# Kernel tuning notes

Hardware: AMD Instinct MI355X
Metric: run time of the kernel (lower is better)

## Reference

```python
import jax, jax.numpy as jnp
import numpy as np

N_QUBITS = 4 + 4  # 8
N_LAYERS = 4
DIM = 2 ** N_QUBITS


def _apply_1q(state, U, wire):
    # state: (B, 2,...,2) complex; U: (2,2) complex; contract qubit `wire`
    s = jnp.moveaxis(state, wire + 1, -1)
    s = s @ U.T  # out[..., i] = sum_j U[i, j] * s[..., j]
    return jnp.moveaxis(s, -1, wire + 1)


def _apply_cnot(state, c, t):
    s = jnp.moveaxis(state, (c + 1, t + 1), (-2, -1))  # (..., 2c, 2t)
    s = jnp.concatenate([s[..., 0:1, :], s[..., 1:2, ::-1]], axis=-2)
    return jnp.moveaxis(s, (-2, -1), (c + 1, t + 1))


def _quantum_layer(q_in, qw):
    """Batched statevector sim: RY(pi*x) encoding + StronglyEntanglingLayers + <Z_i>."""
    B = q_in.shape[0]
    # RY(a)|0> = cos(a/2)|0> + sin(a/2)|1>, a = pi * x  -> product state
    half = q_in * (jnp.pi / 2)
    qvecs = jnp.stack([jnp.cos(half), jnp.sin(half)], axis=-1).astype(jnp.complex64)  # (B, n, 2)
    state = qvecs[:, 0]
    for i in range(1, N_QUBITS):
        state = (state[:, :, None] * qvecs[:, i][:, None, :]).reshape(B, -1)
    state = state.reshape((B,) + (2,) * N_QUBITS)
    # Rot(phi, theta, omega) = RZ(omega) RY(theta) RZ(phi)
    phi, theta, omega = qw[..., 0], qw[..., 1], qw[..., 2]
    c, s = jnp.cos(theta / 2), jnp.sin(theta / 2)
    m00 = jnp.exp(-0.5j * (phi + omega)) * c
    m01 = -jnp.exp(0.5j * (phi - omega)) * s
    m10 = jnp.exp(-0.5j * (phi - omega)) * s
    m11 = jnp.exp(0.5j * (phi + omega)) * c
    rot = jnp.stack([jnp.stack([m00, m01], -1), jnp.stack([m10, m11], -1)], -2)  # (L, n, 2, 2)
    rot = rot.astype(jnp.complex64)
    for l in range(N_LAYERS):
        for w in range(N_QUBITS):
            state = _apply_1q(state, rot[l, w], w)
        r = (l % (N_QUBITS - 1)) + 1  # PennyLane default ranges
        for w in range(N_QUBITS):
            state = _apply_cnot(state, w, (w + r) % N_QUBITS)
    amps = state.reshape(B, DIM)
    probs = jnp.real(amps * jnp.conj(amps))  # (B, 2^n) float32
    # <Z_i> = sum_b probs_b * (+1 if bit_i(b)==0 else -1); wire 0 = most significant axis
    idx = np.arange(DIM)
    bits = (idx[None, :] >> (N_QUBITS - 1 - np.arange(N_QUBITS))[:, None]) & 1  # (n, 2^n)
    zvals = jnp.asarray(1.0 - 2.0 * bits, dtype=jnp.float32)
    return probs @ zvals.T  # (B, n)


def _forward(x, w_pre1, b_pre1, w_pre2, b_pre2, w_pre3, b_pre3, qw,
             w_post1, b_post1, w_post2, b_post2, w_post3, b_post3):
    # eval mode: dropout is identity
    h = jax.nn.relu(x @ w_pre1 + b_pre1)
    h = jax.nn.relu(h @ w_pre2 + b_pre2)
    q_in = jnp.tanh(h @ w_pre3 + b_pre3)          # (B, n_qubits)
    z = _quantum_layer(q_in, qw)                   # (B, n_qubits)
    h = jax.nn.relu(z @ w_post1 + b_post1)
    h = jax.nn.relu(h @ w_post2 + b_post2)
    return h @ w_post3 + b_post3                   # (B, num_classes)


def setup_inputs() -> dict:
    key = jax.random.key(0)
    ks = jax.random.split(key, 16)
    B, D_IN, C = 16384, 41, 5
    def lin(k, fan_in, fan_out):
        lim = 1.0 / np.sqrt(fan_in)
        k1, k2 = jax.random.split(k)
        return (jax.random.uniform(k1, (fan_in, fan_out), jnp.float32, -lim, lim),
                jax.random.uniform(k2, (fan_out,), jnp.float32, -lim, lim))
    x = jax.random.normal(ks[0], (B, D_IN), jnp.float32)
    w_pre1, b_pre1 = lin(ks[1], D_IN, 64)
    w_pre2, b_pre2 = lin(ks[2], 64, 32)
    w_pre3, b_pre3 = lin(ks[3], 32, N_QUBITS)
    qw = jax.random.normal(ks[4], (N_LAYERS, N_QUBITS, 3), jnp.float32) * 0.1
    w_post1, b_post1 = lin(ks[5], N_QUBITS, 32)
    w_post2, b_post2 = lin(ks[6], 32, 16)
    w_post3, b_post3 = lin(ks[7], 16, C)
    return dict(x=x, w_pre1=w_pre1, b_pre1=b_pre1, w_pre2=w_pre2, b_pre2=b_pre2,
                w_pre3=w_pre3, b_pre3=b_pre3, qw=qw,
                w_post1=w_post1, b_post1=b_post1, w_post2=w_post2, b_post2=b_post2,
                w_post3=w_post3, b_post3=b_post3)


def reference(x, w_pre1, b_pre1, w_pre2, b_pre2, w_pre3, b_pre3, qw,
              w_post1, b_post1, w_post2, b_post2, w_post3, b_post3):
    return _forward(x, w_pre1, b_pre1, w_pre2, b_pre2, w_pre3, b_pre3, qw,
                    w_post1, b_post1, w_post2, b_post2, w_post3, b_post3)
```

## Files before the change

kernel.cpp:

```cpp
#include <hip/hip_runtime.h>
#include <math.h>

#define PI_HALF 1.57079632679489662f

typedef float v2f __attribute__((ext_vector_type(2)));
typedef _Float16 h8 __attribute__((ext_vector_type(8)));
typedef _Float16 h2v __attribute__((ext_vector_type(2)));
typedef float f4 __attribute__((ext_vector_type(4)));


__device__ __forceinline__ v2f sp(float x) { v2f r; r.x = x; r.y = x; return r; }
__device__ __forceinline__ v2f pkfma(v2f a, v2f b, v2f c) {
  return __builtin_elementwise_fma(a, b, c);
}

template <int CTRL>
__device__ __forceinline__ float dpp_mov(float v) {
  int r = __builtin_amdgcn_update_dpp(0, __float_as_int(v), CTRL, 0xf, 0xf, true);
  return __int_as_float(r);
}
template <int CTRL, int ROW, int BANK>
__device__ __forceinline__ float mdpp(float old_, float src) {
  int r = __builtin_amdgcn_update_dpp(__float_as_int(old_), __float_as_int(src),
                                      CTRL, ROW, BANK, false);
  return __int_as_float(r);
}
template <int MASK>
__device__ __forceinline__ float lane_xor(float v) {
  if constexpr (MASK == 1) return dpp_mov<0xB1>(v);
  else if constexpr (MASK == 2) return dpp_mov<0x4E>(v);
  else if constexpr (MASK == 8) return dpp_mov<0x128>(v);
  else return dpp_mov<0x1B>(dpp_mov<0x141>(v));
}
template <int MASK>
__device__ __forceinline__ v2f dpp2(v2f v) {
  v2f r; r.x = lane_xor<MASK>(v.x); r.y = lane_xor<MASK>(v.y); return r;
}

template <int W>
__device__ __forceinline__ void rot_lane(v2f (&RE)[8], v2f (&IM)[8],
                                         const float4 mA, int g) {
  constexpr int LM = 1 << (3 - W);
  const unsigned bit = (g >> (3 - W)) & 1u;
  const int sgn = (int)(bit << 31);
  v2f Av = sp(mA.x);
  v2f Bv = sp(__int_as_float(__float_as_int(mA.y) ^ sgn));
  v2f Cv = sp(__int_as_float(__float_as_int(mA.z) ^ sgn));
  v2f Dv = sp(mA.w);
#pragma unroll
  for (int j = 0; j < 8; ++j) {
    v2f pr = dpp2<LM>(RE[j]);
    v2f pi = dpp2<LM>(IM[j]);
    v2f nr = pkfma(-Dv, pi, pkfma(Cv, pr, pkfma(-Bv, IM[j], Av * RE[j])));
    v2f ni = pkfma( Dv, pr, pkfma(Cv, pi, pkfma( Bv, RE[j], Av * IM[j])));
    RE[j] = nr; IM[j] = ni;
  }
}
template <int JM>
__device__ __forceinline__ void rot_regj(v2f (&RE)[8], v2f (&IM)[8],
                                         const float4 mA) {
  v2f M0r = sp(mA.x), M0i = sp(mA.y), M1r = sp(mA.z), M1i = sp(mA.w);
#pragma unroll
  for (int j = 0; j < 8; ++j) {
    if (!(j & JM)) {
      const int j1 = j | JM;
      v2f r0 = RE[j], i0 = IM[j], r1 = RE[j1], i1 = IM[j1];
      RE[j]  = pkfma(-M1i, i1, pkfma(M1r, r1, pkfma(-M0i, i0, M0r * r0)));
      IM[j]  = pkfma( M1i, r1, pkfma(M1r, i1, pkfma( M0i, r0, M0r * i0)));
      RE[j1] = pkfma( M0i, i1, pkfma(M0r, r1, pkfma(-M1i, i0, (-M1r) * r0)));
      IM[j1] = pkfma(-M0i, r1, pkfma(M0r, i1, pkfma( M1i, r0, (-M1r) * i0)));
    }
  }
}
__device__ __forceinline__ void rot_regh(v2f (&RE)[8], v2f (&IM)[8],
                                         const float4 mA) {
#pragma unroll
  for (int j = 0; j < 8; ++j) {
    float r0 = RE[j].x, i0 = IM[j].x, r1 = RE[j].y, i1 = IM[j].y;
    RE[j].x = fmaf(-mA.w, i1, fmaf(mA.z, r1, fmaf(-mA.y, i0, mA.x * r0)));
    IM[j].x = fmaf( mA.w, r1, fmaf(mA.z, i1, fmaf( mA.y, r0, mA.x * i0)));
    RE[j].y = fmaf( mA.y, i1, fmaf(mA.x, r1, fmaf(-mA.w, i0, -mA.z * r0)));
    IM[j].y = fmaf(-mA.y, r1, fmaf(mA.x, i1, fmaf( mA.w, r0, -mA.z * i0)));
  }
}
template <int GPOS, int LM>
__device__ __forceinline__ void cnot_LL(v2f (&RE)[8], v2f (&IM)[8], int g) {
  if constexpr (GPOS >= 2) {
    constexpr int BANK = (GPOS == 3) ? 0xC : 0xA;
    if constexpr (LM == 4) {
#pragma unroll
      for (int j = 0; j < 8; ++j) {
        float t0 = dpp_mov<0x141>(RE[j].x);
        float t1 = dpp_mov<0x141>(RE[j].y);
        float t2 = dpp_mov<0x141>(IM[j].x);
        float t3 = dpp_mov<0x141>(IM[j].y);
        RE[j].x = mdpp<0x1B, 0xF, BANK>(RE[j].x, t0);
        RE[j].y = mdpp<0x1B, 0xF, BANK>(RE[j].y, t1);
        IM[j].x = mdpp<0x1B, 0xF, BANK>(IM[j].x, t2);
        IM[j].y = mdpp<0x1B, 0xF, BANK>(IM[j].y, t3);
      }
    } else {
      constexpr int CTRL = (LM == 1) ? 0xB1 : (LM == 2) ? 0x4E : 0x128;
#pragma unroll
      for (int j = 0; j < 8; ++j) {
        RE[j].x = mdpp<CTRL, 0xF, BANK>(RE[j].x, RE[j].x);
        RE[j].y = mdpp<CTRL, 0xF, BANK>(RE[j].y, RE[j].y);
        IM[j].x = mdpp<CTRL, 0xF, BANK>(IM[j].x, IM[j].x);
        IM[j].y = mdpp<CTRL, 0xF, BANK>(IM[j].y, IM[j].y);
      }
    }
  } else {
    constexpr int CTRL =
        (GPOS == 1 && LM == 1) ? 0xB4 :
        (GPOS == 1 && LM == 2) ? 0x44 :
        (GPOS == 0 && LM == 1) ? 0xA0 :
                                 0x6C;
#pragma unroll
    for (int j = 0; j < 8; ++j) {
      RE[j].x = dpp_mov<CTRL>(RE[j].x);
      RE[j].y = dpp_mov<CTRL>(RE[j].y);
      IM[j].x = dpp_mov<CTRL>(IM[j].x);
      IM[j].y = dpp_mov<CTRL>(IM[j].y);
    }
  }
}
template <int GPOS, int JM>
__device__ __forceinline__ void cnot_LR(v2f (&RE)[8], v2f (&IM)[8], int g) {
  const bool cb = (g >> GPOS) & 1;
#pragma unroll
  for (int j = 0; j < 8; ++j) {
    if (!(j & JM)) {
      const int j1 = j | JM;
      v2f r0 = RE[j], r1 = RE[j1];
      RE[j] = cb ? r1 : r0;  RE[j1] = cb ? r0 : r1;
      v2f i0 = IM[j], i1 = IM[j1];
      IM[j] = cb ? i1 : i0;  IM[j1] = cb ? i0 : i1;
    }
  }
}
template <int GPOS>
__device__ __forceinline__ void cnot_LH(v2f (&RE)[8], v2f (&IM)[8], int g) {
  const bool cb = (g >> GPOS) & 1;
#pragma unroll
  for (int j = 0; j < 8; ++j) {
    v2f r = RE[j]; v2f rs; rs.x = r.y; rs.y = r.x;
    RE[j] = cb ? rs : r;
    v2f i = IM[j]; v2f is2; is2.x = i.y; is2.y = i.x;
    IM[j] = cb ? is2 : i;
  }
}
template <int JC, int LM>
__device__ __forceinline__ void cnot_RL(v2f (&RE)[8], v2f (&IM)[8]) {
#pragma unroll
  for (int j = 0; j < 8; ++j) {
    if (j & JC) {
      RE[j] = dpp2<LM>(RE[j]);
      IM[j] = dpp2<LM>(IM[j]);
    }
  }
}
template <int JC>
__device__ __forceinline__ void cnot_RH(v2f (&RE)[8], v2f (&IM)[8]) {
#pragma unroll
  for (int j = 0; j < 8; ++j) {
    if (j & JC) {
      v2f r = RE[j]; RE[j].x = r.y; RE[j].y = r.x;
      v2f i = IM[j]; IM[j].x = i.y; IM[j].y = i.x;
    }
  }
}
template <int LM>
__device__ __forceinline__ void cnot_HL(v2f (&RE)[8], v2f (&IM)[8]) {
#pragma unroll
  for (int j = 0; j < 8; ++j) {
    RE[j].y = lane_xor<LM>(RE[j].y);
    IM[j].y = lane_xor<LM>(IM[j].y);
  }
}
template <int JC, int JT>
__device__ __forceinline__ void cnot_RR(v2f (&RE)[8], v2f (&IM)[8]) {
#pragma unroll
  for (int j = 0; j < 8; ++j) {
    if ((j & JC) && !(j & JT)) {
      const int j1 = j | JT;
      v2f t = RE[j]; RE[j] = RE[j1]; RE[j1] = t;
      t = IM[j]; IM[j] = IM[j1]; IM[j1] = t;
    }
  }
}

__device__ __forceinline__ void stage_fence() { __threadfence_block(); }

#define CIRCUIT_BODY(RE, IM, g)                                        \
  ROTS(0)                                                              \
  cnot_LL<3, 4>(RE, IM, g);  cnot_LL<2, 2>(RE, IM, g);                 \
  cnot_LL<1, 1>(RE, IM, g);  cnot_LR<0, 4>(RE, IM, g);                 \
  cnot_RR<4, 2>(RE, IM);     cnot_RR<2, 1>(RE, IM);                    \
  cnot_RH<1>(RE, IM);        cnot_HL<8>(RE, IM);                       \
  ROTS(1)                                                              \
  cnot_LL<3, 2>(RE, IM, g);  cnot_LL<2, 1>(RE, IM, g);                 \
  cnot_LR<1, 4>(RE, IM, g);  cnot_LR<0, 2>(RE, IM, g);                 \
  cnot_RR<4, 1>(RE, IM);     cnot_RH<2>(RE, IM);                       \
  cnot_RL<1, 8>(RE, IM);     cnot_HL<4>(RE, IM);                       \
  ROTS(2)                                                              \
  cnot_LL<3, 1>(RE, IM, g);  cnot_LR<2, 4>(RE, IM, g);                 \
  cnot_LR<1, 2>(RE, IM, g);  cnot_LR<0, 1>(RE, IM, g);                 \
  cnot_RH<4>(RE, IM);        cnot_RL<2, 8>(RE, IM);                    \
  cnot_RL<1, 4>(RE, IM);     cnot_HL<2>(RE, IM);                       \
  ROTS(3)                                                              \
  cnot_LR<3, 4>(RE, IM, g);  cnot_LR<2, 2>(RE, IM, g);                 \
  cnot_LR<1, 1>(RE, IM, g);  cnot_LH<0>(RE, IM, g);                    \
  cnot_RL<4, 8>(RE, IM);     cnot_RL<2, 4>(RE, IM);                    \
  cnot_RL<1, 2>(RE, IM);     cnot_HL<1>(RE, IM);

__global__ __launch_bounds__(256) void build_u_kernel(
    const float* __restrict__ qw, _Float16* __restrict__ Btf) {
  __shared__ __align__(16) float rotm[32][4];
  const int tid = threadIdx.x;
  const int g = tid & 15;
  const int ls = tid >> 4;
  const int c = blockIdx.x * 16 + ls;

  if (tid < 32) {
    float phi = qw[tid * 3 + 0];
    float th  = qw[tid * 3 + 1];
    float om  = qw[tid * 3 + 2];
    float st_, ct; sincosf(0.5f * th, &st_, &ct);
    float sa, ca;  sincosf(0.5f * (phi + om), &sa, &ca);
    float sb, cb;  sincosf(0.5f * (phi - om), &sb, &cb);
    rotm[tid][0] =  ca * ct;
    rotm[tid][1] = -sa * ct;
    rotm[tid][2] = -cb * st_;
    rotm[tid][3] = -sb * st_;
  }
  __syncthreads();

  v2f RE[8], IM[8];
#pragma unroll
  for (int j = 0; j < 8; ++j) {
    RE[j].x = (c == g * 16 + 2 * j)     ? 1.0f : 0.0f;
    RE[j].y = (c == g * 16 + 2 * j + 1) ? 1.0f : 0.0f;
    IM[j] = sp(0.0f);
  }

#define RM(L, W) (*(const float4*)(&rotm[(L) * 8 + (W)][0]))
#define ROTS(L)                                                          \
  {                                                                      \
    float4 c0 = RM(L, 0), c1 = RM(L, 1), c2 = RM(L, 2), c3 = RM(L, 3),   \
           c4 = RM(L, 4), c5 = RM(L, 5), c6 = RM(L, 6), c7 = RM(L, 7);   \
    rot_lane<0>(RE, IM, c0, g);                                          \
    rot_lane<1>(RE, IM, c1, g);                                          \
    rot_lane<2>(RE, IM, c2, g);                                          \
    rot_lane<3>(RE, IM, c3, g);                                          \
    rot_regj<4>(RE, IM, c4);                                             \
    rot_regj<2>(RE, IM, c5);                                             \
    rot_regj<1>(RE, IM, c6);                                             \
    rot_regh(RE, IM, c7);                                                \
  }
  CIRCUIT_BODY(RE, IM, g)
#undef ROTS
#undef RM

  {
    const int kt = c >> 5;
    const int rg = (c >> 3) & 3;
    const int e  = c & 7;
    const int baseR = ((g * 2 + 0) * 8 + kt) * 512 + rg * 128 + e;
    const int baseI = ((g * 2 + 1) * 8 + kt) * 512 + rg * 128 + e;
#pragma unroll
    for (int j = 0; j < 8; ++j) {
      Btf[baseR + (2 * j) * 8]     = (_Float16)RE[j].x;
      Btf[baseR + (2 * j + 1) * 8] = (_Float16)RE[j].y;
      Btf[baseI + (2 * j) * 8]     = (_Float16)IM[j].x;
      Btf[baseI + (2 * j + 1) * 8] = (_Float16)IM[j].y;
    }
  }
}

__global__ __launch_bounds__(256) void hqc_main(
    const float* __restrict__ x,
    const float* __restrict__ w1, const float* __restrict__ b1,
    const float* __restrict__ w2, const float* __restrict__ b2,
    const float* __restrict__ w3, const float* __restrict__ b3,
    const _Float16* __restrict__ Btf,
    const float* __restrict__ wp1, const float* __restrict__ bp1,
    const float* __restrict__ wp2, const float* __restrict__ bp2,
    const float* __restrict__ wp3, const float* __restrict__ bp3,
    float* __restrict__ out, int B) {
  __shared__ __align__(16) _Float16 A_half[4096];
  __shared__ __align__(16) float R1[16][44];
  __shared__ __align__(16) float R2[16][68];

  const int tid = threadIdx.x;
  const int g = tid & 15;
  const int ls = tid >> 4;
  const int s = blockIdx.x * 16 + ls;
  const bool valid = (s < B);

  if (valid) {
    R1[ls][g]      = x[s * 41 + g];
    R1[ls][g + 16] = x[s * 41 + g + 16];
    if (g < 9) R1[ls][g + 32] = x[s * 41 + g + 32];
  }
  stage_fence();

  {
    const float4* w1v = (const float4*)w1;
    float4 bv = ((const float4*)b1)[g];
    v2f aA; aA.x = bv.x; aA.y = bv.y;
    v2f aB; aB.x = bv.z; aB.y = bv.w;
#pragma unroll 8
    for (int k = 0; k < 41; ++k) {
      float xk = R1[ls][k];
      float4 wv = w1v[k * 16 + g];
      v2f w01; w01.x = wv.x; w01.y = wv.y;
      v2f w23; w23.x = wv.z; w23.y = wv.w;
      v2f xv = sp(xk);
      aA = pkfma(xv, w01, aA);
      aB = pkfma(xv, w23, aB);
    }
    float4 st4;
    st4.x = fmaxf(aA.x, 0.f); st4.y = fmaxf(aA.y, 0.f);
    st4.z = fmaxf(aB.x, 0.f); st4.w = fmaxf(aB.y, 0.f);
    *(float4*)(&R2[ls][4 * g]) = st4;
  }
  stage_fence();

  {
    const v2f* w2v = (const v2f*)w2;
    v2f a2 = ((const v2f*)b2)[g];
#pragma unroll 8
    for (int k = 0; k < 64; ++k)
      a2 = pkfma(sp(R2[ls][k]), w2v[k * 16 + g], a2);
    R1[ls][2 * g]     = fmaxf(a2.x, 0.f);
    R1[ls][2 * g + 1] = fmaxf(a2.y, 0.f);
  }
  stage_fence();

  if (g < 8) {
    float acc = b3[g];
#pragma unroll
    for (int k = 0; k < 32; ++k) acc = fmaf(R1[ls][k], w3[k * 8 + g], acc);
    float q = tanhf(acc);
    float sh, ch; sincosf(q * PI_HALF, &sh, &ch);
    R2[ls][g]     = ch;
    R2[ls][8 + g] = sh;
  }
  stage_fence();

  {
    float cwv[8], swv[8];
#pragma unroll
    for (int w = 0; w < 8; ++w) { cwv[w] = R2[ls][w]; swv[w] = R2[ls][8 + w]; }
    float lp = 1.0f;
#pragma unroll
    for (int w = 0; w < 4; ++w) lp *= ((g >> (3 - w)) & 1) ? swv[w] : cwv[w];
    float f45[4];
#pragma unroll
    for (int a = 0; a < 4; ++a)
      f45[a] = ((a & 2) ? swv[4] : cwv[4]) * ((a & 1) ? swv[5] : cwv[5]);
    v2f F67[2];
    F67[0].x = cwv[6] * cwv[7]; F67[0].y = cwv[6] * swv[7];
    F67[1].x = swv[6] * cwv[7]; F67[1].y = swv[6] * swv[7];
#pragma unroll
    for (int j = 0; j < 8; ++j) {
      v2f amp = sp(lp * f45[j >> 1]) * F67[j & 1];
      h2v pk; pk.x = (_Float16)amp.x; pk.y = (_Float16)amp.y;
      const int k = g * 16 + 2 * j;
      const int addr = ((k >> 5) * 4 + ((k >> 3) & 3)) * 128 + ls * 8 + (k & 7);
      *(h2v*)(&A_half[addr]) = pk;
    }
  }
  __syncthreads();

  {
    const int l = tid & 63;
    const int w = tid >> 6;

    f4 accr[4], acci[4];
#pragma unroll
    for (int t = 0; t < 4; ++t) {
      accr[t] = (f4){0.f, 0.f, 0.f, 0.f};
      acci[t] = (f4){0.f, 0.f, 0.f, 0.f};
    }
    const _Float16* Arow = &A_half[l * 8];
    const _Float16* Bre[4];
    const _Float16* Bim[4];
#pragma unroll
    for (int t = 0; t < 4; ++t) {
      const int p = w + 4 * t;
      Bre[t] = Btf + ((p * 2 + 0) * 8) * 512 + l * 8;
      Bim[t] = Btf + ((p * 2 + 1) * 8) * 512 + l * 8;
    }

#pragma unroll
    for (int kt = 0; kt < 8; ++kt) {
      h8 av = *(const h8*)(Arow + kt * 512);
      h8 br0 = *(const h8*)(Bre[0] + kt * 512);
      h8 bi0 = *(const h8*)(Bim[0] + kt * 512);
      h8 br1 = *(const h8*)(Bre[1] + kt * 512);
      h8 bi1 = *(const h8*)(Bim[1] + kt * 512);
      h8 br2 = *(const h8*)(Bre[2] + kt * 512);
      h8 bi2 = *(const h8*)(Bim[2] + kt * 512);
      h8 br3 = *(const h8*)(Bre[3] + kt * 512);
      h8 bi3 = *(const h8*)(Bim[3] + kt * 512);
      accr[0] = __builtin_amdgcn_mfma_f32_16x16x32_f16(av, br0, accr[0], 0, 0, 0);
      acci[0] = __builtin_amdgcn_mfma_f32_16x16x32_f16(av, bi0, acci[0], 0, 0, 0);
      accr[1] = __builtin_amdgcn_mfma_f32_16x16x32_f16(av, br1, accr[1], 0, 0, 0);
      acci[1] = __builtin_amdgcn_mfma_f32_16x16x32_f16(av, bi1, acci[1], 0, 0, 0);
      accr[2] = __builtin_amdgcn_mfma_f32_16x16x32_f16(av, br2, accr[2], 0, 0, 0);
      acci[2] = __builtin_amdgcn_mfma_f32_16x16x32_f16(av, bi2, acci[2], 0, 0, 0);
      accr[3] = __builtin_amdgcn_mfma_f32_16x16x32_f16(av, br3, accr[3], 0, 0, 0);
      acci[3] = __builtin_amdgcn_mfma_f32_16x16x32_f16(av, bi3, acci[3], 0, 0, 0);
    }

    const int cN = l & 15;
    const int rgrp = l >> 4;
    float4 zlo[4], zhi[4];
#pragma unroll
    for (int v = 0; v < 4; ++v) {
      zlo[v] = make_float4(0.f, 0.f, 0.f, 0.f);
      zhi[v] = make_float4(0.f, 0.f, 0.f, 0.f);
    }
    const float4 csgn = make_float4((cN & 8) ? -1.f : 1.f, (cN & 4) ? -1.f : 1.f,
                                    (cN & 2) ? -1.f : 1.f, (cN & 1) ? -1.f : 1.f);
#pragma unroll
    for (int t = 0; t < 4; ++t) {
      const int p = w + 4 * t;
      const float4 psgn = make_float4((p & 8) ? -1.f : 1.f, (p & 4) ? -1.f : 1.f,
                                      (p & 2) ? -1.f : 1.f, (p & 1) ? -1.f : 1.f);
#pragma unroll
      for (int v = 0; v < 4; ++v) {
        float tot = fmaf(accr[t][v], accr[t][v], acci[t][v] * acci[t][v]);
        zlo[v].x = fmaf(tot, psgn.x, zlo[v].x);
        zlo[v].y = fmaf(tot, psgn.y, zlo[v].y);
        zlo[v].z = fmaf(tot, psgn.z, zlo[v].z);
        zlo[v].w = fmaf(tot, psgn.w, zlo[v].w);
        zhi[v].x = fmaf(tot, csgn.x, zhi[v].x);
        zhi[v].y = fmaf(tot, csgn.y, zhi[v].y);
        zhi[v].z = fmaf(tot, csgn.z, zhi[v].z);
        zhi[v].w = fmaf(tot, csgn.w, zhi[v].w);
      }
    }

#define RED(M)                                                            \
  _Pragma("unroll")                                                       \
  for (int v = 0; v < 4; ++v) {                                           \
    zlo[v].x += lane_xor<M>(zlo[v].x); zlo[v].y += lane_xor<M>(zlo[v].y); \
    zlo[v].z += lane_xor<M>(zlo[v].z); zlo[v].w += lane_xor<M>(zlo[v].w); \
    zhi[v].x += lane_xor<M>(zhi[v].x); zhi[v].y += lane_xor<M>(zhi[v].y); \
    zhi[v].z += lane_xor<M>(zhi[v].z); zhi[v].w += lane_xor<M>(zhi[v].w); \
  }
    RED(1) RED(2) RED(4) RED(8)
#undef RED

    if (cN == 0) {
#pragma unroll
      for (int v = 0; v < 4; ++v) {
        const int smp = rgrp * 4 + v;
        *(float4*)&R1[smp][w * 8]     = zlo[v];
        *(float4*)&R1[smp][w * 8 + 4] = zhi[v];
      }
    }
  }
  __syncthreads();

  float zp[8];
#pragma unroll
  for (int k = 0; k < 8; ++k)
    zp[k] = (R1[ls][k] + R1[ls][8 + k]) + (R1[ls][16 + k] + R1[ls][24 + k]);

  {
    const v2f* wp1v = (const v2f*)wp1;
    v2f q1 = ((const v2f*)bp1)[g];
#pragma unroll
    for (int k = 0; k < 8; ++k)
      q1 = pkfma(sp(zp[k]), wp1v[k * 16 + g], q1);
    R2[ls][2 * g]     = fmaxf(q1.x, 0.f);
    R2[ls][2 * g + 1] = fmaxf(q1.y, 0.f);
  }
  stage_fence();

  {
    float q2 = bp2[g];
#pragma unroll
    for (int k = 0; k < 32; ++k) q2 = fmaf(R2[ls][k], wp2[k * 16 + g], q2);
    R1[ls][g] = fmaxf(q2, 0.f);
  }
  stage_fence();

  if (g < 5 && valid) {
    float o = bp3[g];
#pragma unroll
    for (int k = 0; k < 16; ++k) o = fmaf(R1[ls][k], wp3[k * 5 + g], o);
    out[s * 5 + g] = o;
  }
}

extern "C" void kernel_launch(void* const* d_in, const int* in_sizes, int n_in,
                              void* d_out, int out_size, void* d_ws,
                              size_t ws_size, hipStream_t stream) {
  const float* x   = (const float*)d_in[0];
  const float* w1  = (const float*)d_in[1];
  const float* b1  = (const float*)d_in[2];
  const float* w2  = (const float*)d_in[3];
  const float* b2  = (const float*)d_in[4];
  const float* w3  = (const float*)d_in[5];
  const float* b3  = (const float*)d_in[6];
  const float* qw  = (const float*)d_in[7];
  const float* wp1 = (const float*)d_in[8];
  const float* bp1 = (const float*)d_in[9];
  const float* wp2 = (const float*)d_in[10];
  const float* bp2 = (const float*)d_in[11];
  const float* wp3 = (const float*)d_in[12];
  const float* bp3 = (const float*)d_in[13];
  float* out = (float*)d_out;
  _Float16* Btf = (_Float16*)d_ws;
  const int B = in_sizes[0] / 41;

  hipLaunchKernelGGL(build_u_kernel, dim3(16), dim3(256), 0, stream, qw, Btf);

  const int blocks = (B + 15) / 16;
  hipLaunchKernelGGL(hqc_main, dim3(blocks), dim3(256), 0, stream,
                     x, w1, b1, w2, b2, w3, b3, Btf,
                     wp1, bp1, wp2, bp2, wp3, bp3, out, B);
}
```

Before: 44.97 us.

## Split fused main kernel into prep, GEMM and post-MLP kernels

Breaks the single fused kernel into three launches: one builds the fp16 product-state amplitudes into a global workspace, one runs the MFMA GEMM with the circuit unitary and reduces the <Z> partials to global memory, and one runs the post-MLP. The apparent aim is to lower per-kernel register and LDS pressure and improve occupancy for each phase. In exchange it adds two kernel launches and global-memory round trips for the amplitudes and partial sums, and the A operand is now read from global memory rather than LDS.

```diff
diff --git a/kernel.cpp b/kernel.cpp
--- a/kernel.cpp
+++ b/kernel.cpp
@@ -277,17 +277,12 @@
   }
 }
 
-__global__ __launch_bounds__(256) void hqc_main(
+__global__ __launch_bounds__(256) void psi_prep(
     const float* __restrict__ x,
     const float* __restrict__ w1, const float* __restrict__ b1,
     const float* __restrict__ w2, const float* __restrict__ b2,
     const float* __restrict__ w3, const float* __restrict__ b3,
-    const _Float16* __restrict__ Btf,
-    const float* __restrict__ wp1, const float* __restrict__ bp1,
-    const float* __restrict__ wp2, const float* __restrict__ bp2,
-    const float* __restrict__ wp3, const float* __restrict__ bp3,
-    float* __restrict__ out, int B) {
-  __shared__ __align__(16) _Float16 A_half[4096];
+    _Float16* __restrict__ Af, int B) {
   __shared__ __align__(16) float R1[16][44];
   __shared__ __align__(16) float R2[16][68];
 
@@ -348,7 +343,7 @@
   }
   stage_fence();
 
-  {
+  if (valid) {
     float cwv[8], swv[8];
 #pragma unroll
     for (int w = 0; w < 8; ++w) { cwv[w] = R2[ls][w]; swv[w] = R2[ls][8 + w]; }
@@ -362,86 +357,92 @@
     v2f F67[2];
     F67[0].x = cwv[6] * cwv[7]; F67[0].y = cwv[6] * swv[7];
     F67[1].x = swv[6] * cwv[7]; F67[1].y = swv[6] * swv[7];
+    _Float16* Ag = Af + (size_t)blockIdx.x * 4096;
 #pragma unroll
     for (int j = 0; j < 8; ++j) {
       v2f amp = sp(lp * f45[j >> 1]) * F67[j & 1];
       h2v pk; pk.x = (_Float16)amp.x; pk.y = (_Float16)amp.y;
       const int k = g * 16 + 2 * j;
       const int addr = ((k >> 5) * 4 + ((k >> 3) & 3)) * 128 + ls * 8 + (k & 7);
-      *(h2v*)(&A_half[addr]) = pk;
-    }
-  }
-  __syncthreads();
-
-  {
-    const int l = tid & 63;
-    const int w = tid >> 6;
-
-    f4 accr[4], acci[4];
-#pragma unroll
-    for (int t = 0; t < 4; ++t) {
-      accr[t] = (f4){0.f, 0.f, 0.f, 0.f};
-      acci[t] = (f4){0.f, 0.f, 0.f, 0.f};
-    }
-    const _Float16* Arow = &A_half[l * 8];
-    const _Float16* Bre[4];
-    const _Float16* Bim[4];
-#pragma unroll
-    for (int t = 0; t < 4; ++t) {
-      const int p = w + 4 * t;
-      Bre[t] = Btf + ((p * 2 + 0) * 8) * 512 + l * 8;
-      Bim[t] = Btf + ((p * 2 + 1) * 8) * 512 + l * 8;
-    }
-
-#pragma unroll
-    for (int kt = 0; kt < 8; ++kt) {
-      h8 av = *(const h8*)(Arow + kt * 512);
-      h8 br0 = *(const h8*)(Bre[0] + kt * 512);
-      h8 bi0 = *(const h8*)(Bim[0] + kt * 512);
-      h8 br1 = *(const h8*)(Bre[1] + kt * 512);
-      h8 bi1 = *(const h8*)(Bim[1] + kt * 512);
-      h8 br2 = *(const h8*)(Bre[2] + kt * 512);
-      h8 bi2 = *(const h8*)(Bim[2] + kt * 512);
-      h8 br3 = *(const h8*)(Bre[3] + kt * 512);
-      h8 bi3 = *(const h8*)(Bim[3] + kt * 512);
-      accr[0] = __builtin_amdgcn_mfma_f32_16x16x32_f16(av, br0, accr[0], 0, 0, 0);
-      acci[0] = __builtin_amdgcn_mfma_f32_16x16x32_f16(av, bi0, acci[0], 0, 0, 0);
-      accr[1] = __builtin_amdgcn_mfma_f32_16x16x32_f16(av, br1, accr[1], 0, 0, 0);
-      acci[1] = __builtin_amdgcn_mfma_f32_16x16x32_f16(av, bi1, acci[1], 0, 0, 0);
-      accr[2] = __builtin_amdgcn_mfma_f32_16x16x32_f16(av, br2, accr[2], 0, 0, 0);
-      acci[2] = __builtin_amdgcn_mfma_f32_16x16x32_f16(av, bi2, acci[2], 0, 0, 0);
-      accr[3] = __builtin_amdgcn_mfma_f32_16x16x32_f16(av, br3, accr[3], 0, 0, 0);
-      acci[3] = __builtin_amdgcn_mfma_f32_16x16x32_f16(av, bi3, acci[3], 0, 0, 0);
-    }
-
-    const int cN = l & 15;
-    const int rgrp = l >> 4;
-    float4 zlo[4], zhi[4];
+      *(h2v*)(&Ag[addr]) = pk;
+    }
+  }
+}
+
+__global__ __launch_bounds__(256) void zgemm_kernel(
+    const _Float16* __restrict__ Btf, const _Float16* __restrict__ Af,
+    float* __restrict__ zpart, int B) {
+  const int tid = threadIdx.x;
+  const int l = tid & 63;
+  const int w = tid >> 6;
+
+  const _Float16* Ag = Af + (size_t)blockIdx.x * 4096;
+
+  f4 accr[4], acci[4];
+#pragma unroll
+  for (int t = 0; t < 4; ++t) {
+    accr[t] = (f4){0.f, 0.f, 0.f, 0.f};
+    acci[t] = (f4){0.f, 0.f, 0.f, 0.f};
+  }
+  const _Float16* Arow = Ag + l * 8;
+  const _Float16* Bre[4];
+  const _Float16* Bim[4];
+#pragma unroll
+  for (int t = 0; t < 4; ++t) {
+    const int p = w + 4 * t;
+    Bre[t] = Btf + ((p * 2 + 0) * 8) * 512 + l * 8;
+    Bim[t] = Btf + ((p * 2 + 1) * 8) * 512 + l * 8;
+  }
+
+#pragma unroll
+  for (int kt = 0; kt < 8; ++kt) {
+    h8 av = *(const h8*)(Arow + kt * 512);
+    h8 br0 = *(const h8*)(Bre[0] + kt * 512);
+    h8 bi0 = *(const h8*)(Bim[0] + kt * 512);
+    h8 br1 = *(const h8*)(Bre[1] + kt * 512);
+    h8 bi1 = *(const h8*)(Bim[1] + kt * 512);
+    h8 br2 = *(const h8*)(Bre[2] + kt * 512);
+    h8 bi2 = *(const h8*)(Bim[2] + kt * 512);
+    h8 br3 = *(const h8*)(Bre[3] + kt * 512);
+    h8 bi3 = *(const h8*)(Bim[3] + kt * 512);
+    accr[0] = __builtin_amdgcn_mfma_f32_16x16x32_f16(av, br0, accr[0], 0, 0, 0);
+    acci[0] = __builtin_amdgcn_mfma_f32_16x16x32_f16(av, bi0, acci[0], 0, 0, 0);
+    accr[1] = __builtin_amdgcn_mfma_f32_16x16x32_f16(av, br1, accr[1], 0, 0, 0);
+    acci[1] = __builtin_amdgcn_mfma_f32_16x16x32_f16(av, bi1, acci[1], 0, 0, 0);
+    accr[2] = __builtin_amdgcn_mfma_f32_16x16x32_f16(av, br2, accr[2], 0, 0, 0);
+    acci[2] = __builtin_amdgcn_mfma_f32_16x16x32_f16(av, bi2, acci[2], 0, 0, 0);
+    accr[3] = __builtin_amdgcn_mfma_f32_16x16x32_f16(av, br3, accr[3], 0, 0, 0);
+    acci[3] = __builtin_amdgcn_mfma_f32_16x16x32_f16(av, bi3, acci[3], 0, 0, 0);
+  }
+
+  const int cN = l & 15;
+  const int rgrp = l >> 4;
+  float4 zlo[4], zhi[4];
+#pragma unroll
+  for (int v = 0; v < 4; ++v) {
+    zlo[v] = make_float4(0.f, 0.f, 0.f, 0.f);
+    zhi[v] = make_float4(0.f, 0.f, 0.f, 0.f);
+  }
+  const float4 csgn = make_float4((cN & 8) ? -1.f : 1.f, (cN & 4) ? -1.f : 1.f,
+                                  (cN & 2) ? -1.f : 1.f, (cN & 1) ? -1.f : 1.f);
+#pragma unroll
+  for (int t = 0; t < 4; ++t) {
+    const int p = w + 4 * t;
+    const float4 psgn = make_float4((p & 8) ? -1.f : 1.f, (p & 4) ? -1.f : 1.f,
+                                    (p & 2) ? -1.f : 1.f, (p & 1) ? -1.f : 1.f);
 #pragma unroll
     for (int v = 0; v < 4; ++v) {
-      zlo[v] = make_float4(0.f, 0.f, 0.f, 0.f);
-      zhi[v] = make_float4(0.f, 0.f, 0.f, 0.f);
-    }
-    const float4 csgn = make_float4((cN & 8) ? -1.f : 1.f, (cN & 4) ? -1.f : 1.f,
-                                    (cN & 2) ? -1.f : 1.f, (cN & 1) ? -1.f : 1.f);
-#pragma unroll
-    for (int t = 0; t < 4; ++t) {
-      const int p = w + 4 * t;
-      const float4 psgn = make_float4((p & 8) ? -1.f : 1.f, (p & 4) ? -1.f : 1.f,
-                                      (p & 2) ? -1.f : 1.f, (p & 1) ? -1.f : 1.f);
-#pragma unroll
-      for (int v = 0; v < 4; ++v) {
-        float tot = fmaf(accr[t][v], accr[t][v], acci[t][v] * acci[t][v]);
-        zlo[v].x = fmaf(tot, psgn.x, zlo[v].x);
-        zlo[v].y = fmaf(tot, psgn.y, zlo[v].y);
-        zlo[v].z = fmaf(tot, psgn.z, zlo[v].z);
-        zlo[v].w = fmaf(tot, psgn.w, zlo[v].w);
-        zhi[v].x = fmaf(tot, csgn.x, zhi[v].x);
-        zhi[v].y = fmaf(tot, csgn.y, zhi[v].y);
-        zhi[v].z = fmaf(tot, csgn.z, zhi[v].z);
-        zhi[v].w = fmaf(tot, csgn.w, zhi[v].w);
-      }
-    }
+      float tot = fmaf(accr[t][v], accr[t][v], acci[t][v] * acci[t][v]);
+      zlo[v].x = fmaf(tot, psgn.x, zlo[v].x);
+      zlo[v].y = fmaf(tot, psgn.y, zlo[v].y);
+      zlo[v].z = fmaf(tot, psgn.z, zlo[v].z);
+      zlo[v].w = fmaf(tot, psgn.w, zlo[v].w);
+      zhi[v].x = fmaf(tot, csgn.x, zhi[v].x);
+      zhi[v].y = fmaf(tot, csgn.y, zhi[v].y);
+      zhi[v].z = fmaf(tot, csgn.z, zhi[v].z);
+      zhi[v].w = fmaf(tot, csgn.w, zhi[v].w);
+    }
+  }
 
 #define RED(M)                                                            \
   _Pragma("unroll")                                                       \
@@ -451,24 +452,40 @@
     zhi[v].x += lane_xor<M>(zhi[v].x); zhi[v].y += lane_xor<M>(zhi[v].y); \
     zhi[v].z += lane_xor<M>(zhi[v].z); zhi[v].w += lane_xor<M>(zhi[v].w); \
   }
-    RED(1) RED(2) RED(4) RED(8)
+  RED(1) RED(2) RED(4) RED(8)
 #undef RED
 
-    if (cN == 0) {
-#pragma unroll
-      for (int v = 0; v < 4; ++v) {
-        const int smp = rgrp * 4 + v;
-        *(float4*)&R1[smp][w * 8]     = zlo[v];
-        *(float4*)&R1[smp][w * 8 + 4] = zhi[v];
-      }
-    }
-  }
-  __syncthreads();
-
+  if (cN == 0) {
+#pragma unroll
+    for (int v = 0; v < 4; ++v) {
+      const int smp = rgrp * 4 + v;
+      const size_t s = (size_t)blockIdx.x * 16 + smp;
+      *(float4*)&zpart[s * 32 + w * 8]     = zlo[v];
+      *(float4*)&zpart[s * 32 + w * 8 + 4] = zhi[v];
+    }
+  }
+}
+
+__global__ __launch_bounds__(256) void post_kernel(
+    const float* __restrict__ zpart,
+    const float* __restrict__ wp1, const float* __restrict__ bp1,
+    const float* __restrict__ wp2, const float* __restrict__ bp2,
+    const float* __restrict__ wp3, const float* __restrict__ bp3,
+    float* __restrict__ out, int B) {
+  __shared__ float P1[16][34];
+  __shared__ float P2[16][18];
+
+  const int tid = threadIdx.x;
+  const int g = tid & 15;
+  const int ls = tid >> 4;
+  const int s = blockIdx.x * 16 + ls;
+  const bool valid = (s < B);
+
+  const float* zrow = zpart + (size_t)s * 32;
   float zp[8];
 #pragma unroll
   for (int k = 0; k < 8; ++k)
-    zp[k] = (R1[ls][k] + R1[ls][8 + k]) + (R1[ls][16 + k] + R1[ls][24 + k]);
+    zp[k] = (zrow[k] + zrow[8 + k]) + (zrow[16 + k] + zrow[24 + k]);
 
   {
     const v2f* wp1v = (const v2f*)wp1;
@@ -476,23 +493,23 @@
 #pragma unroll
     for (int k = 0; k < 8; ++k)
       q1 = pkfma(sp(zp[k]), wp1v[k * 16 + g], q1);
-    R2[ls][2 * g]     = fmaxf(q1.x, 0.f);
-    R2[ls][2 * g + 1] = fmaxf(q1.y, 0.f);
+    P1[ls][2 * g]     = fmaxf(q1.x, 0.f);
+    P1[ls][2 * g + 1] = fmaxf(q1.y, 0.f);
   }
   stage_fence();
 
   {
     float q2 = bp2[g];
 #pragma unroll
-    for (int k = 0; k < 32; ++k) q2 = fmaf(R2[ls][k], wp2[k * 16 + g], q2);
-    R1[ls][g] = fmaxf(q2, 0.f);
+    for (int k = 0; k < 32; ++k) q2 = fmaf(P1[ls][k], wp2[k * 16 + g], q2);
+    P2[ls][g] = fmaxf(q2, 0.f);
   }
   stage_fence();
 
   if (g < 5 && valid) {
     float o = bp3[g];
 #pragma unroll
-    for (int k = 0; k < 16; ++k) o = fmaf(R1[ls][k], wp3[k * 5 + g], o);
+    for (int k = 0; k < 16; ++k) o = fmaf(P2[ls][k], wp3[k * 5 + g], o);
     out[s * 5 + g] = o;
   }
 }
@@ -515,13 +532,22 @@
   const float* wp3 = (const float*)d_in[12];
   const float* bp3 = (const float*)d_in[13];
   float* out = (float*)d_out;
-  _Float16* Btf = (_Float16*)d_ws;
   const int B = in_sizes[0] / 41;
 
+  char* ws = (char*)d_ws;
+  _Float16* Btf  = (_Float16*)ws;
+  _Float16* Af   = (_Float16*)(ws + (256 << 10));
+  float*    zprt = (float*)(ws + (256 << 10) + ((size_t)B * 512));
+
   hipLaunchKernelGGL(build_u_kernel, dim3(16), dim3(256), 0, stream, qw, Btf);
 
-  const int blocks = (B + 15) / 16;
-  hipLaunchKernelGGL(hqc_main, dim3(blocks), dim3(256), 0, stream,
-                     x, w1, b1, w2, b2, w3, b3, Btf,
-                     wp1, bp1, wp2, bp2, wp3, bp3, out, B);
-}
+  const int g16 = (B + 15) / 16;
+  hipLaunchKernelGGL(psi_prep, dim3(g16), dim3(256), 0, stream,
+                     x, w1, b1, w2, b2, w3, b3, Af, B);
+
+  hipLaunchKernelGGL(zgemm_kernel, dim3(g16), dim3(256), 0, stream,
+                     Btf, Af, zprt, B);
+
+  hipLaunchKernelGGL(post_kernel, dim3(g16), dim3(256), 0, stream,
+                     zprt, wp1, bp1, wp2, bp2, wp3, bp3, out, B);
+}
```

New measurement: 52.66 us. 17.1% more time.
